# Kernel optimization log

Hardware: AMD Instinct MI355X
Metric: run time of the kernel (lower is better)

The kernel has to match this reference:

```python
import jax, jax.numpy as jnp
import numpy as np

B, N, FIN, FOUT, E = 2, 50000, 128, 64, 800000


def setup_inputs() -> dict:
    key = jax.random.key(0)
    ks = jax.random.split(key, 7)
    x = jax.random.normal(ks[0], (B, N, FIN), dtype=jnp.float32)
    W = jax.random.normal(ks[1], (FIN, FOUT), dtype=jnp.float32) * (1.0 / np.sqrt(FIN))
    W_self = jax.random.normal(ks[2], (FIN, FOUT), dtype=jnp.float32) * (1.0 / np.sqrt(FIN))
    b_self = jax.random.normal(ks[3], (FOUT,), dtype=jnp.float32) * 0.01
    edge_row = jax.random.randint(ks[4], (E,), 0, N, dtype=jnp.int32)
    edge_col = jax.random.randint(ks[5], (E,), 0, N, dtype=jnp.int32)
    edge_val = jax.random.uniform(ks[6], (E,), dtype=jnp.float32)
    return {"x": x, "W": W, "W_self": W_self, "b_self": b_self,
            "edge_row": edge_row, "edge_col": edge_col, "edge_val": edge_val}


def reference(x, W, W_self, b_self, edge_row, edge_col, edge_val):
    # x: (B, N, FIN); adjacency in COO form: out[r] += val * in[c]
    Bn, Nn, _ = x.shape
    Fo = W.shape[1]
    x_trans = jnp.einsum("bnf,fo->bno", x, W)               # (B, N, FOUT), no bias
    # Same layout trick as torch: sparse.mm over (N, B*FOUT)
    xr = x_trans.transpose(1, 0, 2).reshape(Nn, Bn * Fo)    # (N, B*FOUT)
    msgs = edge_val[:, None] * xr[edge_col]                  # (E, B*FOUT) gather
    agg = jax.ops.segment_sum(msgs, edge_row, num_segments=Nn)  # (N, B*FOUT) scatter-add
    agg = agg.reshape(Nn, Bn, Fo).transpose(1, 0, 2)         # (B, N, FOUT)
    self_c = jnp.einsum("bnf,fo->bno", x, W_self) + b_self   # Linear with bias
    return jax.nn.relu(self_c + agg)
```

## Files before the change

### kernel.cpp

```cpp
#include <hip/hip_runtime.h>
#include <hip/hip_fp16.h>

#define Bc   2
#define Nn   50000
#define FINc 128
#define FOUTc 64
#define Mtot (Bc * Nn)
#define CCOMB 128
#define GB 1563
#define CAP 64

#define NRNG   128
#define NBUCK  391
#define ABLK   256
#define BCAP   2432
#define FUSED_GRID (ABLK * 9)

typedef __bf16 bf16x8 __attribute__((ext_vector_type(8)));
typedef float  f32x4  __attribute__((ext_vector_type(4)));

static __device__ inline unsigned short f2bf(float f) {
    unsigned int u = __float_as_uint(f);
    u += 0x7fffu + ((u >> 16) & 1u);
    return (unsigned short)(u >> 16);
}

__global__ __launch_bounds__(256) void prep(
    const float* __restrict__ W, const float* __restrict__ Ws,
    unsigned short* __restrict__ Bp, unsigned int* __restrict__ bfill)
{
    if (blockIdx.x < 8) {
        const int idx = blockIdx.x * 256 + threadIdx.x;
        const int lane = idx & 63;
        const int kt   = (idx >> 6) & 3;
        const int nt   = idx >> 8;
        const int n    = nt * 16 + (lane & 15);
        const int k0   = kt * 32 + (lane >> 4) * 8;
        unsigned short o8[8];
#pragma unroll
        for (int j = 0; j < 8; ++j) {
            const int f = k0 + j;
            const float v = (n < 64) ? W[f * FOUTc + n] : Ws[f * FOUTc + (n - 64)];
            o8[j] = f2bf(v);
        }
        *(uint4*)&Bp[(size_t)idx * 8] = *(uint4*)o8;
    } else {
        for (int i = threadIdx.x; i < NBUCK; i += 256) bfill[i] = 0u;
    }
}

__global__ __launch_bounds__(256) void gemm_bina(
    const float* __restrict__ x, const unsigned short* __restrict__ Bp,
    const float* __restrict__ bself,
    unsigned short* __restrict__ xrb, float* __restrict__ outp,
    const int* __restrict__ erow, const int* __restrict__ ecol,
    const float* __restrict__ evalv, unsigned int* __restrict__ bfill,
    uint2* __restrict__ stage, int E, int ec)
{
    const int b  = blockIdx.x;
    const int r9 = b % 9;

    if (r9 == 8) {
        __shared__ unsigned int hist[512];
        __shared__ unsigned int gbase[NBUCK];
        __shared__ unsigned int cur[NBUCK];

        const int tid = threadIdx.x;
        const int ord = b / 9;
        const int e0 = ord * ec;
        int e1 = e0 + ec; if (e1 > E) e1 = E;

        hist[tid] = 0u; hist[tid + 256] = 0u;
        for (int i = tid; i < NBUCK; i += 256) cur[i] = 0u;
        __syncthreads();

        for (int e = e0 + tid; e < e1; e += 256)
            atomicAdd(&hist[erow[e] >> 7], 1u);
        __syncthreads();

        for (int i = tid; i < NBUCK; i += 256) {
            const unsigned int c = hist[i];
            gbase[i] = c ? atomicAdd(&bfill[i], c) : 0u;
        }
        __syncthreads();

        for (int e = e0 + tid; e < e1; e += 256) {
            const int   r = erow[e];
            const int   c = ecol[e];
            const float v = evalv[e];
            const int  nb = r >> 7;
            const unsigned int k = gbase[nb] + atomicAdd(&cur[nb], 1u);
            if (k < BCAP)
                stage[(size_t)nb * BCAP + k] = make_uint2(
                    ((unsigned int)__half_as_ushort(__float2half(v)) << 17) |
                        (unsigned int)c,
                    (unsigned int)(r & 127));
        }
        return;
    }

    const int gb = b - (b + 1) / 9;
    if (gb >= GB) return;
    const int lane = threadIdx.x & 63;
    const int quad = lane >> 4;
    const int mbase = gb * 64 + (threadIdx.x >> 6) * 16;

    const int mrow   = mbase + (lane & 15);
    const int mclamp = (mrow < Mtot) ? mrow : (Mtot - 1);
    const float* __restrict__ xrow = &x[(size_t)mclamp * FINc + quad * 8];

    float4 xv[8];
#pragma unroll
    for (int kt = 0; kt < 4; ++kt) {
        xv[2 * kt]     = *(const float4*)&xrow[kt * 32];
        xv[2 * kt + 1] = *(const float4*)&xrow[kt * 32 + 4];
    }

    f32x4 acc[8] = {};

#pragma unroll
    for (int kt = 0; kt < 4; ++kt) {
        const float4 xa = xv[2 * kt];
        const float4 xb = xv[2 * kt + 1];
        bf16x8 bf;
        bf[0] = (__bf16)xa.x; bf[1] = (__bf16)xa.y;
        bf[2] = (__bf16)xa.z; bf[3] = (__bf16)xa.w;
        bf[4] = (__bf16)xb.x; bf[5] = (__bf16)xb.y;
        bf[6] = (__bf16)xb.z; bf[7] = (__bf16)xb.w;

        const bf16x8* __restrict__ abase =
            (const bf16x8*)&Bp[(size_t)(kt * 64 + lane) * 8];
#pragma unroll
        for (int nt = 0; nt < 8; ++nt) {
            const bf16x8 af = abase[nt * 4 * 64];
            acc[nt] = __builtin_amdgcn_mfma_f32_16x16x32_bf16(af, bf, acc[nt], 0, 0, 0);
        }
    }

    const int m = mbase + (lane & 15);
    if (m < Mtot) {
        const int bb = (m >= Nn) ? 1 : 0;
        const int n = m - bb * Nn;
        unsigned short* __restrict__ xp = &xrb[(size_t)n * CCOMB + bb * FOUTc];
        const int cq = quad * 4;
#pragma unroll
        for (int nt = 0; nt < 4; ++nt) {
            const int c = nt * 16 + cq;
            unsigned short h[4];
            h[0] = f2bf(acc[nt][0]); h[1] = f2bf(acc[nt][1]);
            h[2] = f2bf(acc[nt][2]); h[3] = f2bf(acc[nt][3]);
            *(uint2*)&xp[c] = *(uint2*)h;
        }
        float* __restrict__ op = &outp[(size_t)m * FOUTc];
#pragma unroll
        for (int nt = 4; nt < 8; ++nt) {
            const int o = (nt - 4) * 16 + cq;
            const float4 b4 = *(const float4*)&bself[o];
            float4 v;
            v.x = acc[nt][0] + b4.x; v.y = acc[nt][1] + b4.y;
            v.z = acc[nt][2] + b4.z; v.w = acc[nt][3] + b4.w;
            *(float4*)&op[o] = v;
        }
    }
}

__global__ __launch_bounds__(256) void bin_b(
    const unsigned int* __restrict__ bfill, const uint2* __restrict__ stage,
    unsigned int* __restrict__ cvp, int* __restrict__ cntp)
{
    __shared__ unsigned int lists[NRNG * CAP];
    __shared__ unsigned int lcnt[NRNG];

    const int tid = threadIdx.x;
    const int nb  = blockIdx.x;
    const int row0 = nb << 7;
    int nrows = Nn - row0; if (nrows > NRNG) nrows = NRNG;

    for (int i = tid; i < NRNG; i += 256) lcnt[i] = 0u;
    __syncthreads();

    unsigned int cnt = bfill[nb];
    if (cnt > BCAP) cnt = BCAP;
    const uint2* __restrict__ seg = &stage[(size_t)nb * BCAP];

    for (unsigned int j = tid; j < cnt; j += 256) {
        const uint2 rec = seg[j];
        const int rl = (int)(rec.y & 127u);
        const unsigned int k = atomicAdd(&lcnt[rl], 1u);
        if (k < CAP) lists[(rl << 6) + k] = rec.x;
    }
    __syncthreads();

    unsigned int* __restrict__ dst = &cvp[(size_t)row0 << 6];
    const int words = nrows << 6;
    for (int i = tid; i < words; i += 256) dst[i] = lists[i];
    for (int rl = tid; rl < nrows; rl += 256) {
        const unsigned int c = lcnt[rl];
        cntp[(size_t)(row0 + rl) * 16] = (int)(c < CAP ? c : CAP);
    }
}

#define GATHP(W, PRED, ACC)                                                   \
    {                                                                         \
        const unsigned int w = (W);                                           \
        unsigned int col = w & 0x1FFFFu;                                      \
        col = (col < Nn) ? col : 0u;           \
        const float vv = (PRED) ? __half2float(__ushort_as_half(              \
                             (unsigned short)(w >> 17))) : 0.0f;              \
        const uint4 raw = *(const uint4*)&xrb[(size_t)col * CCOMB + c0];      \
        ACC[0] = fmaf(vv, __uint_as_float(raw.x << 16),         ACC[0]);      \
        ACC[1] = fmaf(vv, __uint_as_float(raw.x & 0xffff0000u), ACC[1]);      \
        ACC[2] = fmaf(vv, __uint_as_float(raw.y << 16),         ACC[2]);      \
        ACC[3] = fmaf(vv, __uint_as_float(raw.y & 0xffff0000u), ACC[3]);      \
        ACC[4] = fmaf(vv, __uint_as_float(raw.z << 16),         ACC[4]);      \
        ACC[5] = fmaf(vv, __uint_as_float(raw.z & 0xffff0000u), ACC[5]);      \
        ACC[6] = fmaf(vv, __uint_as_float(raw.w << 16),         ACC[6]);      \
        ACC[7] = fmaf(vv, __uint_as_float(raw.w & 0xffff0000u), ACC[7]);      \
    }

__global__ __launch_bounds__(256) void row_gather(
    const int* __restrict__ cntp, const unsigned int* __restrict__ cvp,
    const unsigned short* __restrict__ xrb, float* __restrict__ outp)
{
    const int j    = blockIdx.x;
    const int low3 = j & 7;
    const int h    = (low3 >= 4) ? 1 : 0;
    const int ord  = (j >> 3) * 4 + (low3 & 3);
    int n = ord * 4 + (threadIdx.x >> 6);
    n = __builtin_amdgcn_readfirstlane(n);

    const int lane = threadIdx.x & 63;
    const int slot = lane >> 3;
    const int c0   = h * 64 + (lane & 7) * 8;
    const unsigned int* __restrict__ seg = &cvp[(size_t)n << 6];

    const int kc = min(cntp[(size_t)n * 16], CAP);
    const unsigned int u0 = seg[slot];
    const unsigned int u1 = seg[8 + slot];

    float aA[8] = {0.f, 0.f, 0.f, 0.f, 0.f, 0.f, 0.f, 0.f};

    GATHP(u0, slot < kc,     aA);
    GATHP(u1, slot + 8 < kc, aA);

    for (int e = 16 + slot; e < kc; e += 8) {
        const unsigned int u = seg[e];
        GATHP(u, true, aA);
    }

#pragma unroll
    for (int i = 0; i < 8; ++i) {
        aA[i] += __shfl_down(aA[i], 8);
        aA[i] += __shfl_down(aA[i], 16);
        aA[i] += __shfl_down(aA[i], 32);
    }

    if (lane < 8) {
        const size_t m = (size_t)h * Nn + n;
        const int o = lane * 8;
        float* __restrict__ op = &outp[m * FOUTc + o];
        float4 s0 = *(float4*)&op[0];
        float4 s1 = *(float4*)&op[4];
        s0.x = fmaxf(s0.x + aA[0], 0.0f); s0.y = fmaxf(s0.y + aA[1], 0.0f);
        s0.z = fmaxf(s0.z + aA[2], 0.0f); s0.w = fmaxf(s0.w + aA[3], 0.0f);
        s1.x = fmaxf(s1.x + aA[4], 0.0f); s1.y = fmaxf(s1.y + aA[5], 0.0f);
        s1.z = fmaxf(s1.z + aA[6], 0.0f); s1.w = fmaxf(s1.w + aA[7], 0.0f);
        *(float4*)&op[0] = s0;
        *(float4*)&op[4] = s1;
    }
}

extern "C" void kernel_launch(void* const* d_in, const int* in_sizes, int n_in,
                              void* d_out, int out_size, void* d_ws, size_t ws_size,
                              hipStream_t stream)
{
    const float* x    = (const float*)d_in[0];
    const float* W    = (const float*)d_in[1];
    const float* Ws   = (const float*)d_in[2];
    const float* bs   = (const float*)d_in[3];
    const int*   erow = (const int*)d_in[4];
    const int*   ecol = (const int*)d_in[5];
    const float* eval = (const float*)d_in[6];
    float* outp = (float*)d_out;
    const int E = in_sizes[4];

    unsigned short* xrb = (unsigned short*)d_ws;
    unsigned int*   cvp = (unsigned int*)(xrb + (size_t)Nn * CCOMB);
    int*            cntp = (int*)(cvp + ((size_t)Nn << 6));
    unsigned short* Bp  = (unsigned short*)(cntp + (size_t)Nn * 16);
    unsigned int*   bfill = (unsigned int*)(Bp + 16384);
    uint2*          stage = (uint2*)(bfill + 512);

    const int ec = (E + ABLK - 1) / ABLK;

    prep<<<9, 256, 0, stream>>>(W, Ws, Bp, bfill);

    gemm_bina<<<FUSED_GRID, 256, 0, stream>>>(x, Bp, bs, xrb, outp,
                                              erow, ecol, eval, bfill,
                                              stage, E, ec);

    bin_b<<<NBUCK, 256, 0, stream>>>(bfill, stage, cvp, cntp);

    row_gather<<<Nn / 2, 256, 0, stream>>>(cntp, cvp, xrb, outp);
}
```

Baseline: 179.1 us.

## Replace global atomic bucket fill with per-block local sort and coalesced chunk write

The binning blocks no longer reserve slots in global per-bucket counters with atomics and scatter records across buckets. Each block now counting-sorts its edges by bucket in shared memory using a prefix scan, writes its chunk contiguously, and records per-block counts and offsets in matrices. bin_b then has each of its 256 threads read one block's run for its bucket, which removes the global atomics and the bfill zeroing. The cost is serialized per-thread loops in bin_b with uneven run lengths, plus a silent cap of RECCAP edges per block.

```diff
diff --git a/kernel.cpp b/kernel.cpp
--- a/kernel.cpp
+++ b/kernel.cpp
@@ -13,7 +13,7 @@
 #define NRNG   128
 #define NBUCK  391
 #define ABLK   256
-#define BCAP   2432
+#define RECCAP 3200
 #define FUSED_GRID (ABLK * 9)
 
 typedef __bf16 bf16x8 __attribute__((ext_vector_type(8)));
@@ -27,26 +27,22 @@
 
 __global__ __launch_bounds__(256) void prep(
     const float* __restrict__ W, const float* __restrict__ Ws,
-    unsigned short* __restrict__ Bp, unsigned int* __restrict__ bfill)
-{
-    if (blockIdx.x < 8) {
-        const int idx = blockIdx.x * 256 + threadIdx.x;
-        const int lane = idx & 63;
-        const int kt   = (idx >> 6) & 3;
-        const int nt   = idx >> 8;
-        const int n    = nt * 16 + (lane & 15);
-        const int k0   = kt * 32 + (lane >> 4) * 8;
-        unsigned short o8[8];
-#pragma unroll
-        for (int j = 0; j < 8; ++j) {
-            const int f = k0 + j;
-            const float v = (n < 64) ? W[f * FOUTc + n] : Ws[f * FOUTc + (n - 64)];
-            o8[j] = f2bf(v);
-        }
-        *(uint4*)&Bp[(size_t)idx * 8] = *(uint4*)o8;
-    } else {
-        for (int i = threadIdx.x; i < NBUCK; i += 256) bfill[i] = 0u;
-    }
+    unsigned short* __restrict__ Bp)
+{
+    const int idx = blockIdx.x * 256 + threadIdx.x;
+    const int lane = idx & 63;
+    const int kt   = (idx >> 6) & 3;
+    const int nt   = idx >> 8;
+    const int n    = nt * 16 + (lane & 15);
+    const int k0   = kt * 32 + (lane >> 4) * 8;
+    unsigned short o8[8];
+#pragma unroll
+    for (int j = 0; j < 8; ++j) {
+        const int f = k0 + j;
+        const float v = (n < 64) ? W[f * FOUTc + n] : Ws[f * FOUTc + (n - 64)];
+        o8[j] = f2bf(v);
+    }
+    *(uint4*)&Bp[(size_t)idx * 8] = *(uint4*)o8;
 }
 
 __global__ __launch_bounds__(256) void gemm_bina(
@@ -54,33 +50,49 @@
     const float* __restrict__ bself,
     unsigned short* __restrict__ xrb, float* __restrict__ outp,
     const int* __restrict__ erow, const int* __restrict__ ecol,
-    const float* __restrict__ evalv, unsigned int* __restrict__ bfill,
-    uint2* __restrict__ stage, int E, int ec)
+    const float* __restrict__ evalv, unsigned int* __restrict__ cntm,
+    unsigned int* __restrict__ ofsm, uint2* __restrict__ stage,
+    int E, int ec)
 {
     const int b  = blockIdx.x;
     const int r9 = b % 9;
 
     if (r9 == 8) {
         __shared__ unsigned int hist[512];
-        __shared__ unsigned int gbase[NBUCK];
+        __shared__ unsigned int incl[512];
         __shared__ unsigned int cur[NBUCK];
+        __shared__ unsigned int recs[RECCAP * 2];
 
         const int tid = threadIdx.x;
         const int ord = b / 9;
         const int e0 = ord * ec;
         int e1 = e0 + ec; if (e1 > E) e1 = E;
+        if (e1 - e0 > RECCAP) e1 = e0 + RECCAP;
+        const int tot = e1 - e0;
 
         hist[tid] = 0u; hist[tid + 256] = 0u;
-        for (int i = tid; i < NBUCK; i += 256) cur[i] = 0u;
         __syncthreads();
 
         for (int e = e0 + tid; e < e1; e += 256)
             atomicAdd(&hist[erow[e] >> 7], 1u);
         __syncthreads();
 
+        incl[tid] = hist[tid]; incl[tid + 256] = hist[tid + 256];
+        __syncthreads();
+        for (int off = 1; off < 512; off <<= 1) {
+            const unsigned int a0 = (tid >= off) ? incl[tid - off] : 0u;
+            const unsigned int a1 = ((tid + 256) >= off) ? incl[tid + 256 - off] : 0u;
+            __syncthreads();
+            incl[tid] += a0; incl[tid + 256] += a1;
+            __syncthreads();
+        }
+
         for (int i = tid; i < NBUCK; i += 256) {
             const unsigned int c = hist[i];
-            gbase[i] = c ? atomicAdd(&bfill[i], c) : 0u;
+            const unsigned int x0 = incl[i] - c;
+            cur[i] = x0;
+            cntm[(size_t)ord * NBUCK + i] = c;
+            ofsm[(size_t)ord * NBUCK + i] = x0;
         }
         __syncthreads();
 
@@ -89,13 +101,16 @@
             const int   c = ecol[e];
             const float v = evalv[e];
             const int  nb = r >> 7;
-            const unsigned int k = gbase[nb] + atomicAdd(&cur[nb], 1u);
-            if (k < BCAP)
-                stage[(size_t)nb * BCAP + k] = make_uint2(
-                    ((unsigned int)__half_as_ushort(__float2half(v)) << 17) |
-                        (unsigned int)c,
-                    (unsigned int)(r & 127));
-        }
+            const unsigned int k = atomicAdd(&cur[nb], 1u);
+            recs[2 * k]     = ((unsigned int)__half_as_ushort(__float2half(v)) << 17) |
+                              (unsigned int)c;
+            recs[2 * k + 1] = (unsigned int)(r & 127);
+        }
+        __syncthreads();
+
+        uint2* __restrict__ chunk = &stage[(size_t)ord * RECCAP];
+        for (int j = tid; j < tot; j += 256)
+            chunk[j] = make_uint2(recs[2 * j], recs[2 * j + 1]);
         return;
     }
 
@@ -165,7 +180,8 @@
 }
 
 __global__ __launch_bounds__(256) void bin_b(
-    const unsigned int* __restrict__ bfill, const uint2* __restrict__ stage,
+    const unsigned int* __restrict__ cntm, const unsigned int* __restrict__ ofsm,
+    const uint2* __restrict__ stage,
     unsigned int* __restrict__ cvp, int* __restrict__ cntp)
 {
     __shared__ unsigned int lists[NRNG * CAP];
@@ -179,15 +195,16 @@
     for (int i = tid; i < NRNG; i += 256) lcnt[i] = 0u;
     __syncthreads();
 
-    unsigned int cnt = bfill[nb];
-    if (cnt > BCAP) cnt = BCAP;
-    const uint2* __restrict__ seg = &stage[(size_t)nb * BCAP];
-
-    for (unsigned int j = tid; j < cnt; j += 256) {
-        const uint2 rec = seg[j];
-        const int rl = (int)(rec.y & 127u);
-        const unsigned int k = atomicAdd(&lcnt[rl], 1u);
-        if (k < CAP) lists[(rl << 6) + k] = rec.x;
+    {
+        const unsigned int c = cntm[(size_t)tid * NBUCK + nb];
+        const unsigned int o = ofsm[(size_t)tid * NBUCK + nb];
+        const uint2* __restrict__ run = &stage[(size_t)tid * RECCAP + o];
+        for (unsigned int j = 0; j < c; ++j) {
+            const uint2 rec = run[j];
+            const int rl = (int)(rec.y & 127u);
+            const unsigned int k = atomicAdd(&lcnt[rl], 1u);
+            if (k < CAP) lists[(rl << 6) + k] = rec.x;
+        }
     }
     __syncthreads();
 
@@ -288,18 +305,19 @@
     unsigned int*   cvp = (unsigned int*)(xrb + (size_t)Nn * CCOMB);
     int*            cntp = (int*)(cvp + ((size_t)Nn << 6));
     unsigned short* Bp  = (unsigned short*)(cntp + (size_t)Nn * 16);
-    unsigned int*   bfill = (unsigned int*)(Bp + 16384);
-    uint2*          stage = (uint2*)(bfill + 512);
+    unsigned int*   cntm = (unsigned int*)(Bp + 16384);
+    unsigned int*   ofsm = cntm + (size_t)ABLK * NBUCK;
+    uint2*          stage = (uint2*)(ofsm + (size_t)ABLK * NBUCK);
 
     const int ec = (E + ABLK - 1) / ABLK;
 
-    prep<<<9, 256, 0, stream>>>(W, Ws, Bp, bfill);
+    prep<<<8, 256, 0, stream>>>(W, Ws, Bp);
 
     gemm_bina<<<FUSED_GRID, 256, 0, stream>>>(x, Bp, bs, xrb, outp,
-                                              erow, ecol, eval, bfill,
-                                              stage, E, ec);
-
-    bin_b<<<NBUCK, 256, 0, stream>>>(bfill, stage, cvp, cntp);
+                                              erow, ecol, eval,
+                                              cntm, ofsm, stage, E, ec);
+
+    bin_b<<<NBUCK, 256, 0, stream>>>(cntm, ofsm, stage, cvp, cntp);
 
     row_gather<<<Nn / 2, 256, 0, stream>>>(cntp, cvp, xrb, outp);
 }
```

Result: no change. 178.4 us (-0.4%).
